# Kernel optimization log

Hardware: AMD Instinct MI355X
Metric: run time of the kernel (lower is better)

## Reference

```python
import jax, jax.numpy as jnp
import numpy as np

B, T, D = 16, 3000, 512
GROUPS, NUM_VARS = 2, 320
VQ_DIM = 256
VAR_DIM = VQ_DIM // GROUPS  # 128


def setup_inputs() -> dict:
    key = jax.random.key(0)
    k_x, k_w, k_v = jax.random.split(key, 3)
    x = jax.random.normal(k_x, (B, T, D), dtype=jnp.float32)
    # weight_proj: Linear(dim, groups*num_vars), weight ~ N(0,1), bias = 0
    W = jax.random.normal(k_w, (GROUPS * NUM_VARS, D), dtype=jnp.float32)
    b = jnp.zeros((GROUPS * NUM_VARS,), dtype=jnp.float32)
    # codebook: nn.init.uniform_ -> U[0,1); combine_groups=False -> num_groups = GROUPS
    codebook = jax.random.uniform(k_v, (1, GROUPS * NUM_VARS, VAR_DIM), dtype=jnp.float32)
    return {"x": x, "W": W, "b": b, "codebook": codebook}


def reference(x, W, b, codebook):
    """Eval-mode GumbelVectorQuantizer forward (hard argmax path).

    Returns (quantized [B,T,VQ_DIM], avg_probs [GROUPS, NUM_VARS]).
    """
    Bv, Tv, Dv = x.shape
    N = Bv * Tv
    # weight_proj
    logits = jnp.einsum('nd,vd->nv', x.reshape(N, Dv), W) + b  # [N, G*V]
    logits = logits.reshape(N, GROUPS, NUM_VARS)
    # hard one-hot over codebook entries per group
    k = jnp.argmax(logits, axis=-1)                             # [N, G] int
    hard = jax.nn.one_hot(k, NUM_VARS, dtype=logits.dtype)      # [N, G, V]
    # avg probs (softmax in fp32, mean over tokens)
    avg_probs = jax.nn.softmax(logits.astype(jnp.float32), axis=-1).mean(axis=0)  # [G, V]
    # dense multiply-sum against codebook == gather of selected code vectors
    vars_g = codebook.reshape(GROUPS, NUM_VARS, VAR_DIM)        # [G, V, d]
    out = jnp.einsum('ngv,gvd->ngd', hard, vars_g)              # [N, G, d]
    out = out.reshape(Bv, Tv, GROUPS * VAR_DIM)                 # [B, T, VQ_DIM]
    return out, avg_probs
```

## Files before the change

kernel.cpp:

```cpp
#include <hip/hip_runtime.h>

#define GROUPS 2
#define NUM_VARS 320
#define NVT 640
#define DIM 512
#define VAR_DIM 128
#define NTOK 48000
#define TM 32
#define TMF 64
#define BLOCK 256
#define KCH 256
#define XP 264
#define NT16 40
#define NKS 16
#define NTILE (NTOK / 16)
#define TSTRIDE (NKS * 2 * 512)

typedef short bf16x8 __attribute__((ext_vector_type(8)));
typedef float f32x4  __attribute__((ext_vector_type(4)));
typedef unsigned short u16;
typedef u16 u16x4 __attribute__((ext_vector_type(4)));
typedef u16 u16x8 __attribute__((ext_vector_type(8)));

__device__ inline u16 bf16_rne(float f) {
    unsigned u = __builtin_bit_cast(unsigned, f);
    return (u16)((u + 0x7fffu + ((u >> 16) & 1u)) >> 16);
}
__device__ inline void split2(float f, u16& h, u16& l) {
    h = bf16_rne(f);
    float fh = __builtin_bit_cast(float, (unsigned)h << 16);
    l = bf16_rne(f - fh);
}

__global__ void pack_w_kernel(const float* __restrict__ W, u16* __restrict__ Wpk) {
    int idx = blockIdx.x * blockDim.x + threadIdx.x;
    if (idx >= NT16 * NKS * 64 * 8) return;
    int j    = idx & 7;
    int lane = (idx >> 3) & 63;
    int ks   = (idx >> 9) & 15;
    int v16  = idx >> 13;
    int row  = v16 * 16 + (lane & 15);
    int k    = ks * 32 + 8 * (lane >> 4) + j;
    u16 h, l;
    split2(W[(size_t)row * DIM + k], h, l);
    size_t base = (size_t)((v16 * NKS + ks) * 2) * 512 + lane * 8 + j;
    Wpk[base]       = h;
    Wpk[base + 512] = l;
}

__global__ void split_x_pack_kernel(const float* __restrict__ x,
                                    u16* __restrict__ xpk) {
    const int gw   = (blockIdx.x * blockDim.x + threadIdx.x) >> 6;
    const int lane = threadIdx.x & 63;
    if (gw >= NTILE) return;
    const int l15 = lane & 15, l4 = lane >> 4;
    const float* xr = x + (size_t)(gw * 16 + l15) * DIM + 8 * l4;
    u16* dst = xpk + (size_t)gw * TSTRIDE + lane * 8;
#pragma unroll 4
    for (int ks = 0; ks < NKS; ++ks) {
        float4 a = *(const float4*)(xr + ks * 32);
        float4 b = *(const float4*)(xr + ks * 32 + 4);
        u16x8 hv, lv; u16 h, l;
        split2(a.x, h, l); hv[0] = h; lv[0] = l;
        split2(a.y, h, l); hv[1] = h; lv[1] = l;
        split2(a.z, h, l); hv[2] = h; lv[2] = l;
        split2(a.w, h, l); hv[3] = h; lv[3] = l;
        split2(b.x, h, l); hv[4] = h; lv[4] = l;
        split2(b.y, h, l); hv[5] = h; lv[5] = l;
        split2(b.z, h, l); hv[6] = h; lv[6] = l;
        split2(b.w, h, l); hv[7] = h; lv[7] = l;
        *(u16x8*)(dst + ks * 1024)       = hv;
        *(u16x8*)(dst + ks * 1024 + 512) = lv;
    }
}

__global__ __launch_bounds__(BLOCK, 2)
void vq_mfma_reg_kernel(const float* __restrict__ x,
                        const float* __restrict__ W,
                        const u16* __restrict__ xpk,
                        const u16* __restrict__ Wpk,
                        const float* __restrict__ bias,
                        const float* __restrict__ codebook,
                        float* __restrict__ out,
                        float* __restrict__ avg_out) {
    __shared__ float avg_s[NUM_VARS];
    __shared__ float tv_s[TMF][4][2];
    __shared__ int   ti_s[TMF][4][2];
    __shared__ float m_s[TMF], gap_s[TMF], sum_s[TMF];
    __shared__ int   i1_s[TMF], i2_s[TMF], kb_s[TMF];

    const int tid  = threadIdx.x;
    const int lane = tid & 63;
    const int ty   = tid >> 6;
    const int l15  = lane & 15;
    const int l4   = lane >> 4;
    const int g    = blockIdx.x & 1;
    const int n0   = (blockIdx.x >> 1) * TMF;

    for (int i = tid; i < NUM_VARS; i += BLOCK) avg_s[i] = 0.f;

    const f32x4 zf = {0.f, 0.f, 0.f, 0.f};
    f32x4 acc[4][5];
#pragma unroll
    for (int rt = 0; rt < 4; ++rt)
#pragma unroll
        for (int ct = 0; ct < 5; ++ct) acc[rt][ct] = zf;

    const u16* xa = xpk + (size_t)((blockIdx.x >> 1) * 4) * TSTRIDE + lane * 8;
    const u16* wpk_b = Wpk + (size_t)(g * 20 + ty * 5) * TSTRIDE + lane * 8;

#pragma unroll 2
    for (int ks = 0; ks < NKS; ++ks) {
        bf16x8 ah[4], al[4];
#pragma unroll
        for (int rt = 0; rt < 4; ++rt) {
            ah[rt] = *(const bf16x8*)(xa + (size_t)rt * TSTRIDE + ks * 1024);
            al[rt] = *(const bf16x8*)(xa + (size_t)rt * TSTRIDE + ks * 1024 + 512);
        }
#pragma unroll
        for (int ct = 0; ct < 5; ++ct) {
            const u16* wp = wpk_b + (size_t)(ct * NKS + ks) * 2 * 512;
            bf16x8 bh = *(const bf16x8*)wp;
            bf16x8 bl = *(const bf16x8*)(wp + 512);
#pragma unroll
            for (int rt = 0; rt < 4; ++rt) {
                acc[rt][ct] = __builtin_amdgcn_mfma_f32_16x16x32_bf16(ah[rt], bh, acc[rt][ct], 0, 0, 0);
                acc[rt][ct] = __builtin_amdgcn_mfma_f32_16x16x32_bf16(ah[rt], bl, acc[rt][ct], 0, 0, 0);
                acc[rt][ct] = __builtin_amdgcn_mfma_f32_16x16x32_bf16(al[rt], bh, acc[rt][ct], 0, 0, 0);
            }
        }
    }

#pragma unroll
    for (int ct = 0; ct < 5; ++ct) {
        float bv = bias[g * NUM_VARS + ty * 80 + ct * 16 + l15];
#pragma unroll
        for (int rt = 0; rt < 4; ++rt)
#pragma unroll
            for (int j = 0; j < 4; ++j) acc[rt][ct][j] += bv;
    }

#pragma unroll
    for (int rt = 0; rt < 4; ++rt)
#pragma unroll
    for (int j = 0; j < 4; ++j) {
        float v1 = -3.4e38f, v2 = -3.4e38f;
        int   i1 = 0x7fffffff, i2 = 0x7fffffff;
#pragma unroll
        for (int ct = 0; ct < 5; ++ct) {
            float val = acc[rt][ct][j];
            int   vi  = ty * 80 + ct * 16 + l15;
            if ((val > v1) || (val == v1 && vi < i1)) { v2 = v1; i2 = i1; v1 = val; i1 = vi; }
            else if ((val > v2) || (val == v2 && vi < i2)) { v2 = val; i2 = vi; }
        }
#pragma unroll
        for (int off = 1; off <= 8; off <<= 1) {
            float o1 = __shfl_xor(v1, off); int oi1 = __shfl_xor(i1, off);
            float o2 = __shfl_xor(v2, off); int oi2 = __shfl_xor(i2, off);
            if ((o1 > v1) || (o1 == v1 && oi1 < i1)) { v2 = v1; i2 = i1; v1 = o1; i1 = oi1; }
            else if ((o1 > v2) || (o1 == v2 && oi1 < i2)) { v2 = o1; i2 = oi1; }
            if ((o2 > v1) || (o2 == v1 && oi2 < i1)) { v2 = v1; i2 = i1; v1 = o2; i1 = oi2; }
            else if ((o2 > v2) || (o2 == v2 && oi2 < i2)) { v2 = o2; i2 = oi2; }
        }
        if (l15 == 0) {
            const int T = rt * 16 + l4 * 4 + j;
            tv_s[T][ty][0] = v1; tv_s[T][ty][1] = v2;
            ti_s[T][ty][0] = i1; ti_s[T][ty][1] = i2;
        }
    }
    __syncthreads();

    if (tid < TMF) {
        float v1 = -3.4e38f, v2 = -3.4e38f;
        int   i1 = 0x7fffffff, i2 = 0x7fffffff;
#pragma unroll
        for (int w = 0; w < 4; ++w)
#pragma unroll
            for (int q = 0; q < 2; ++q) {
                float val = tv_s[tid][w][q]; int vi = ti_s[tid][w][q];
                if ((val > v1) || (val == v1 && vi < i1)) { v2 = v1; i2 = i1; v1 = val; i1 = vi; }
                else if ((val > v2) || (val == v2 && vi < i2)) { v2 = val; i2 = vi; }
            }
        m_s[tid] = v1; gap_s[tid] = v1 - v2;
        i1_s[tid] = i1; i2_s[tid] = i2; kb_s[tid] = i1; sum_s[tid] = 0.f;
    }
    __syncthreads();

#pragma unroll
    for (int rt = 0; rt < 4; ++rt)
#pragma unroll
    for (int j = 0; j < 4; ++j) {
        const int T = rt * 16 + l4 * 4 + j;
        const float m = m_s[T];
        float s = 0.f;
#pragma unroll
        for (int ct = 0; ct < 5; ++ct) {
            float e = expf(acc[rt][ct][j] - m);
            acc[rt][ct][j] = e;
            s += e;
        }
#pragma unroll
        for (int off = 1; off <= 8; off <<= 1) s += __shfl_xor(s, off);
        if (l15 == 0) atomicAdd(&sum_s[T], s);
    }
    __syncthreads();

#pragma unroll
    for (int ct = 0; ct < 5; ++ct) {
        float tot = 0.f;
#pragma unroll
        for (int rt = 0; rt < 4; ++rt)
#pragma unroll
        for (int j = 0; j < 4; ++j) {
            const int T = rt * 16 + l4 * 4 + j;
            float v = acc[rt][ct][j] / sum_s[T];
            v += __shfl_xor(v, 16);
            v += __shfl_xor(v, 32);
            tot += v;
        }
        if (l4 == 0) avg_s[ty * 80 + ct * 16 + l15] += tot;
    }

    for (int t16 = 0; t16 < 16; ++t16) {
        const int T = ty * 16 + t16;
        if (gap_s[T] <= 0.05f) {
            const int i1 = i1_s[T], i2 = i2_s[T];
            const float* xr = x + (size_t)(n0 + T) * DIM;
            const float* w1 = W + (size_t)(g * NUM_VARS + i1) * DIM;
            const float* w2 = W + (size_t)(g * NUM_VARS + i2) * DIM;
            double d1 = 0.0, d2 = 0.0;
            for (int k = lane; k < DIM; k += 64) {
                double xv = (double)xr[k];
                d1 += xv * (double)w1[k];
                d2 += xv * (double)w2[k];
            }
#pragma unroll
            for (int off = 1; off <= 32; off <<= 1) {
                d1 += __shfl_xor(d1, off);
                d2 += __shfl_xor(d2, off);
            }
            d1 += (double)bias[g * NUM_VARS + i1];
            d2 += (double)bias[g * NUM_VARS + i2];
            if (lane == 0)
                kb_s[T] = (d2 > d1 || (d2 == d1 && i2 < i1)) ? i2 : i1;
        }
    }
    __syncthreads();

#pragma unroll
    for (int i = 0; i < 8; ++i) {
        const int f = tid + i * BLOCK;
        const int T = f >> 5, p = f & 31;
        const int kb = kb_s[T];
        float4 cv = *(const float4*)(codebook +
                     (size_t)(g * NUM_VARS + kb) * VAR_DIM + p * 4);
        *(float4*)(out + (size_t)(n0 + T) * (GROUPS * VAR_DIM) + g * VAR_DIM + p * 4) = cv;
    }

    const float scale = 1.f / (float)NTOK;
    for (int i = tid; i < NUM_VARS; i += BLOCK)
        atomicAdd(&avg_out[g * NUM_VARS + i], avg_s[i] * scale);
}

template <bool USE_WQ>
__global__ __launch_bounds__(BLOCK, 2)
void vq_mfma_kernel(const float* __restrict__ x,
                    const float* __restrict__ W,
                    const u16* __restrict__ Wpk,
                    const float* __restrict__ bias,
                    const float* __restrict__ codebook,
                    float* __restrict__ out,
                    float* __restrict__ avg_out) {
    __shared__ u16 xs_hi[TM][XP];
    __shared__ u16 xs_lo[TM][XP];
    __shared__ float avg_s[NUM_VARS];
    __shared__ float tv_s[TM][4][2];
    __shared__ int   ti_s[TM][4][2];
    __shared__ float m_s[TM], gap_s[TM], sum_s[TM];
    __shared__ int   i1_s[TM], i2_s[TM], kb_s[TM];

    const int tid  = threadIdx.x;
    const int lane = tid & 63;
    const int ty   = tid >> 6;
    const int l15  = lane & 15;
    const int l4   = lane >> 4;
    const int g    = blockIdx.x & 1;
    const int n0   = (blockIdx.x >> 1) * TM;

    for (int i = tid; i < NUM_VARS; i += BLOCK) avg_s[i] = 0.f;

    const f32x4 zf = {0.f, 0.f, 0.f, 0.f};
    f32x4 acc[2][5];
#pragma unroll
    for (int rt = 0; rt < 2; ++rt)
#pragma unroll
        for (int ct = 0; ct < 5; ++ct) acc[rt][ct] = zf;

    const int vw = g * NUM_VARS + ty * 80;

    for (int c = 0; c < DIM / KCH; ++c) {
        __syncthreads();
        {
            const int t  = tid >> 3;
            const int kb = (tid & 7) * 4;
            const float* xp = x + (size_t)(n0 + t) * DIM + c * KCH;
#pragma unroll
            for (int i = 0; i < 8; ++i) {
                const int k = kb + i * 32;
                float4 v = *(const float4*)(xp + k);
                u16x4 hv, lv; u16 h, l;
                split2(v.x, h, l); hv[0] = h; lv[0] = l;
                split2(v.y, h, l); hv[1] = h; lv[1] = l;
                split2(v.z, h, l); hv[2] = h; lv[2] = l;
                split2(v.w, h, l); hv[3] = h; lv[3] = l;
                *(u16x4*)&xs_hi[t][k] = hv;
                *(u16x4*)&xs_lo[t][k] = lv;
            }
        }
        __syncthreads();
#pragma unroll
        for (int ks = 0; ks < KCH / 32; ++ks) {
            const int ko = ks * 32 + 8 * l4;
            bf16x8 ah0 = *(const bf16x8*)&xs_hi[l15][ko];
            bf16x8 al0 = *(const bf16x8*)&xs_lo[l15][ko];
            bf16x8 ah1 = *(const bf16x8*)&xs_hi[16 + l15][ko];
            bf16x8 al1 = *(const bf16x8*)&xs_lo[16 + l15][ko];
            const int ksg = c * (KCH / 32) + ks;
#pragma unroll
            for (int ct = 0; ct < 5; ++ct) {
                bf16x8 bh, bl;
                if (USE_WQ) {
                    const int v16g = g * (NUM_VARS / 16) + ty * 5 + ct;
                    const u16* wp = Wpk + (size_t)((v16g * NKS + ksg) * 2) * 512 + lane * 8;
                    bh = *(const bf16x8*)wp;
                    bl = *(const bf16x8*)(wp + 512);
                } else {
                    const int kg = ksg * 32 + 8 * l4;
                    const float* wp = W + (size_t)(vw + ct * 16 + l15) * DIM + kg;
                    float4 wa = *(const float4*)wp;
                    float4 wb = *(const float4*)(wp + 4);
                    u16 h, l;
                    split2(wa.x, h, l); bh[0] = (short)h; bl[0] = (short)l;
                    split2(wa.y, h, l); bh[1] = (short)h; bl[1] = (short)l;
                    split2(wa.z, h, l); bh[2] = (short)h; bl[2] = (short)l;
                    split2(wa.w, h, l); bh[3] = (short)h; bl[3] = (short)l;
                    split2(wb.x, h, l); bh[4] = (short)h; bl[4] = (short)l;
                    split2(wb.y, h, l); bh[5] = (short)h; bl[5] = (short)l;
                    split2(wb.z, h, l); bh[6] = (short)h; bl[6] = (short)l;
                    split2(wb.w, h, l); bh[7] = (short)h; bl[7] = (short)l;
                }
                acc[0][ct] = __builtin_amdgcn_mfma_f32_16x16x32_bf16(ah0, bh, acc[0][ct], 0, 0, 0);
                acc[0][ct] = __builtin_amdgcn_mfma_f32_16x16x32_bf16(ah0, bl, acc[0][ct], 0, 0, 0);
                acc[0][ct] = __builtin_amdgcn_mfma_f32_16x16x32_bf16(al0, bh, acc[0][ct], 0, 0, 0);
                acc[1][ct] = __builtin_amdgcn_mfma_f32_16x16x32_bf16(ah1, bh, acc[1][ct], 0, 0, 0);
                acc[1][ct] = __builtin_amdgcn_mfma_f32_16x16x32_bf16(ah1, bl, acc[1][ct], 0, 0, 0);
                acc[1][ct] = __builtin_amdgcn_mfma_f32_16x16x32_bf16(al1, bh, acc[1][ct], 0, 0, 0);
            }
        }
    }

#pragma unroll
    for (int ct = 0; ct < 5; ++ct) {
        float bv = bias[vw + ct * 16 + l15];
#pragma unroll
        for (int rt = 0; rt < 2; ++rt)
#pragma unroll
            for (int j = 0; j < 4; ++j) acc[rt][ct][j] += bv;
    }

#pragma unroll
    for (int rt = 0; rt < 2; ++rt)
#pragma unroll
    for (int j = 0; j < 4; ++j) {
        float v1 = -3.4e38f, v2 = -3.4e38f;
        int   i1 = 0x7fffffff, i2 = 0x7fffffff;
#pragma unroll
        for (int ct = 0; ct < 5; ++ct) {
            float val = acc[rt][ct][j];
            int   vi  = ty * 80 + ct * 16 + l15;
            if ((val > v1) || (val == v1 && vi < i1)) { v2 = v1; i2 = i1; v1 = val; i1 = vi; }
            else if ((val > v2) || (val == v2 && vi < i2)) { v2 = val; i2 = vi; }
        }
#pragma unroll
        for (int off = 1; off <= 8; off <<= 1) {
            float o1 = __shfl_xor(v1, off); int oi1 = __shfl_xor(i1, off);
            float o2 = __shfl_xor(v2, off); int oi2 = __shfl_xor(i2, off);
            if ((o1 > v1) || (o1 == v1 && oi1 < i1)) { v2 = v1; i2 = i1; v1 = o1; i1 = oi1; }
            else if ((o1 > v2) || (o1 == v2 && oi1 < i2)) { v2 = o1; i2 = oi1; }
            if ((o2 > v1) || (o2 == v1 && oi2 < i1)) { v2 = v1; i2 = i1; v1 = o2; i1 = oi2; }
            else if ((o2 > v2) || (o2 == v2 && oi2 < i2)) { v2 = o2; i2 = oi2; }
        }
        if (l15 == 0) {
            const int T = rt * 16 + l4 * 4 + j;
            tv_s[T][ty][0] = v1; tv_s[T][ty][1] = v2;
            ti_s[T][ty][0] = i1; ti_s[T][ty][1] = i2;
        }
    }
    __syncthreads();

    if (tid < TM) {
        float v1 = -3.4e38f, v2 = -3.4e38f;
        int   i1 = 0x7fffffff, i2 = 0x7fffffff;
#pragma unroll
        for (int w = 0; w < 4; ++w)
#pragma unroll
            for (int q = 0; q < 2; ++q) {
                float val = tv_s[tid][w][q]; int vi = ti_s[tid][w][q];
                if ((val > v1) || (val == v1 && vi < i1)) { v2 = v1; i2 = i1; v1 = val; i1 = vi; }
                else if ((val > v2) || (val == v2 && vi < i2)) { v2 = val; i2 = vi; }
            }
        m_s[tid] = v1; gap_s[tid] = v1 - v2;
        i1_s[tid] = i1; i2_s[tid] = i2; kb_s[tid] = i1; sum_s[tid] = 0.f;
    }
    __syncthreads();

#pragma unroll
    for (int rt = 0; rt < 2; ++rt)
#pragma unroll
    for (int j = 0; j < 4; ++j) {
        const int T = rt * 16 + l4 * 4 + j;
        const float m = m_s[T];
        float s = 0.f;
#pragma unroll
        for (int ct = 0; ct < 5; ++ct) {
            float e = expf(acc[rt][ct][j] - m);
            acc[rt][ct][j] = e;
            s += e;
        }
#pragma unroll
        for (int off = 1; off <= 8; off <<= 1) s += __shfl_xor(s, off);
        if (l15 == 0) atomicAdd(&sum_s[T], s);
    }
    __syncthreads();

#pragma unroll
    for (int ct = 0; ct < 5; ++ct) {
        float tot = 0.f;
#pragma unroll
        for (int rt = 0; rt < 2; ++rt)
#pragma unroll
        for (int j = 0; j < 4; ++j) {
            const int T = rt * 16 + l4 * 4 + j;
            float v = acc[rt][ct][j] / sum_s[T];
            v += __shfl_xor(v, 16);
            v += __shfl_xor(v, 32);
            tot += v;
        }
        if (l4 == 0) avg_s[ty * 80 + ct * 16 + l15] += tot;
    }

    for (int t8 = 0; t8 < 8; ++t8) {
        const int T = ty * 8 + t8;
        if (gap_s[T] <= 0.05f) {
            const int i1 = i1_s[T], i2 = i2_s[T];
            const float* xr = x + (size_t)(n0 + T) * DIM;
            const float* w1 = W + (size_t)(g * NUM_VARS + i1) * DIM;
            const float* w2 = W + (size_t)(g * NUM_VARS + i2) * DIM;
            double d1 = 0.0, d2 = 0.0;
            for (int k = lane; k < DIM; k += 64) {
                double xv = (double)xr[k];
                d1 += xv * (double)w1[k];
                d2 += xv * (double)w2[k];
            }
#pragma unroll
            for (int off = 1; off <= 32; off <<= 1) {
                d1 += __shfl_xor(d1, off);
                d2 += __shfl_xor(d2, off);
            }
            d1 += (double)bias[g * NUM_VARS + i1];
            d2 += (double)bias[g * NUM_VARS + i2];
            if (lane == 0)
                kb_s[T] = (d2 > d1 || (d2 == d1 && i2 < i1)) ? i2 : i1;
        }
    }
    __syncthreads();

#pragma unroll
    for (int i = 0; i < 4; ++i) {
        const int f = tid + i * BLOCK;
        const int T = f >> 5, p = f & 31;
        const int kb = kb_s[T];
        float4 cv = *(const float4*)(codebook +
                     (size_t)(g * NUM_VARS + kb) * VAR_DIM + p * 4);
        *(float4*)(out + (size_t)(n0 + T) * (GROUPS * VAR_DIM) + g * VAR_DIM + p * 4) = cv;
    }

    const float scale = 1.f / (float)NTOK;
    for (int i = tid; i < NUM_VARS; i += BLOCK)
        atomicAdd(&avg_out[g * NUM_VARS + i], avg_s[i] * scale);
}

extern "C" void kernel_launch(void* const* d_in, const int* in_sizes, int n_in,
                              void* d_out, int out_size, void* d_ws, size_t ws_size,
                              hipStream_t stream) {
    const float* x  = (const float*)d_in[0];
    const float* W  = (const float*)d_in[1];
    const float* b  = (const float*)d_in[2];
    const float* cb = (const float*)d_in[3];
    float* out = (float*)d_out;
    float* avg = out + (size_t)NTOK * GROUPS * VAR_DIM;

    hipMemsetAsync(avg, 0, NVT * sizeof(float), stream);

    const size_t wpk_bytes = (size_t)NT16 * NKS * 2 * 512 * sizeof(u16);
    const size_t xpk_bytes = (size_t)NTILE * NKS * 2 * 512 * sizeof(u16);
    const size_t full_bytes = wpk_bytes + xpk_bytes;

    if (ws_size >= full_bytes) {
        u16* Wpk = (u16*)d_ws;
        u16* xpk = (u16*)((char*)d_ws + wpk_bytes);
        pack_w_kernel<<<(NT16 * NKS * 64 * 8 + 255) / 256, 256, 0, stream>>>(W, Wpk);
        split_x_pack_kernel<<<(NTILE + 3) / 4, 256, 0, stream>>>(x, xpk);
        vq_mfma_reg_kernel<<<(NTOK / TMF) * GROUPS, BLOCK, 0, stream>>>(
            x, W, xpk, Wpk, b, cb, out, avg);
    } else if (ws_size >= wpk_bytes) {
        u16* Wpk = (u16*)d_ws;
        pack_w_kernel<<<(NT16 * NKS * 64 * 8 + 255) / 256, 256, 0, stream>>>(W, Wpk);
        vq_mfma_kernel<true><<<(NTOK / TM) * GROUPS, BLOCK, 0, stream>>>(x, W, Wpk, b, cb, out, avg);
    } else {
        vq_mfma_kernel<false><<<(NTOK / TM) * GROUPS, BLOCK, 0, stream>>>(x, W, nullptr, b, cb, out, avg);
    }
}
```

Measured before the change: 200.6 us.

## Double token tile per block to 128 rows and hoist W fragments across row tiles

Result: slower. 300.8 us (+50.0%).

```diff
diff --git a/kernel.cpp b/kernel.cpp
--- a/kernel.cpp
+++ b/kernel.cpp
@@ -7,7 +7,7 @@
 #define VAR_DIM 128
 #define NTOK 48000
 #define TM 32
-#define TMF 64
+#define TMF 128
 #define BLOCK 256
 #define KCH 256
 #define XP 264
@@ -74,7 +74,7 @@
     }
 }
 
-__global__ __launch_bounds__(BLOCK, 2)
+__global__ __launch_bounds__(BLOCK, 1)
 void vq_mfma_reg_kernel(const float* __restrict__ x,
                         const float* __restrict__ W,
                         const u16* __restrict__ xpk,
@@ -100,33 +100,33 @@
     for (int i = tid; i < NUM_VARS; i += BLOCK) avg_s[i] = 0.f;
 
     const f32x4 zf = {0.f, 0.f, 0.f, 0.f};
-    f32x4 acc[4][5];
-#pragma unroll
-    for (int rt = 0; rt < 4; ++rt)
+    f32x4 acc[8][5];
+#pragma unroll
+    for (int rt = 0; rt < 8; ++rt)
 #pragma unroll
         for (int ct = 0; ct < 5; ++ct) acc[rt][ct] = zf;
 
-    const u16* xa = xpk + (size_t)((blockIdx.x >> 1) * 4) * TSTRIDE + lane * 8;
+    const u16* xa = xpk + (size_t)((blockIdx.x >> 1) * 8) * TSTRIDE + lane * 8;
     const u16* wpk_b = Wpk + (size_t)(g * 20 + ty * 5) * TSTRIDE + lane * 8;
 
 #pragma unroll 2
     for (int ks = 0; ks < NKS; ++ks) {
-        bf16x8 ah[4], al[4];
-#pragma unroll
-        for (int rt = 0; rt < 4; ++rt) {
-            ah[rt] = *(const bf16x8*)(xa + (size_t)rt * TSTRIDE + ks * 1024);
-            al[rt] = *(const bf16x8*)(xa + (size_t)rt * TSTRIDE + ks * 1024 + 512);
-        }
+        bf16x8 bh[5], bl[5];
 #pragma unroll
         for (int ct = 0; ct < 5; ++ct) {
-            const u16* wp = wpk_b + (size_t)(ct * NKS + ks) * 2 * 512;
-            bf16x8 bh = *(const bf16x8*)wp;
-            bf16x8 bl = *(const bf16x8*)(wp + 512);
-#pragma unroll
-            for (int rt = 0; rt < 4; ++rt) {
-                acc[rt][ct] = __builtin_amdgcn_mfma_f32_16x16x32_bf16(ah[rt], bh, acc[rt][ct], 0, 0, 0);
-                acc[rt][ct] = __builtin_amdgcn_mfma_f32_16x16x32_bf16(ah[rt], bl, acc[rt][ct], 0, 0, 0);
-                acc[rt][ct] = __builtin_amdgcn_mfma_f32_16x16x32_bf16(al[rt], bh, acc[rt][ct], 0, 0, 0);
+            const u16* wp = wpk_b + (size_t)(ct * NKS + ks) * 1024;
+            bh[ct] = *(const bf16x8*)wp;
+            bl[ct] = *(const bf16x8*)(wp + 512);
+        }
+#pragma unroll
+        for (int rt = 0; rt < 8; ++rt) {
+            bf16x8 ah = *(const bf16x8*)(xa + (size_t)rt * TSTRIDE + ks * 1024);
+            bf16x8 al = *(const bf16x8*)(xa + (size_t)rt * TSTRIDE + ks * 1024 + 512);
+#pragma unroll
+            for (int ct = 0; ct < 5; ++ct) {
+                acc[rt][ct] = __builtin_amdgcn_mfma_f32_16x16x32_bf16(ah, bh[ct], acc[rt][ct], 0, 0, 0);
+                acc[rt][ct] = __builtin_amdgcn_mfma_f32_16x16x32_bf16(ah, bl[ct], acc[rt][ct], 0, 0, 0);
+                acc[rt][ct] = __builtin_amdgcn_mfma_f32_16x16x32_bf16(al, bh[ct], acc[rt][ct], 0, 0, 0);
             }
         }
     }
@@ -135,13 +135,13 @@
     for (int ct = 0; ct < 5; ++ct) {
         float bv = bias[g * NUM_VARS + ty * 80 + ct * 16 + l15];
 #pragma unroll
-        for (int rt = 0; rt < 4; ++rt)
+        for (int rt = 0; rt < 8; ++rt)
 #pragma unroll
             for (int j = 0; j < 4; ++j) acc[rt][ct][j] += bv;
     }
 
 #pragma unroll
-    for (int rt = 0; rt < 4; ++rt)
+    for (int rt = 0; rt < 8; ++rt)
 #pragma unroll
     for (int j = 0; j < 4; ++j) {
         float v1 = -3.4e38f, v2 = -3.4e38f;
@@ -187,7 +187,7 @@
     __syncthreads();
 
 #pragma unroll
-    for (int rt = 0; rt < 4; ++rt)
+    for (int rt = 0; rt < 8; ++rt)
 #pragma unroll
     for (int j = 0; j < 4; ++j) {
         const int T = rt * 16 + l4 * 4 + j;
@@ -195,7 +195,7 @@
         float s = 0.f;
 #pragma unroll
         for (int ct = 0; ct < 5; ++ct) {
-            float e = expf(acc[rt][ct][j] - m);
+            float e = __expf(acc[rt][ct][j] - m);
             acc[rt][ct][j] = e;
             s += e;
         }
@@ -205,24 +205,36 @@
     }
     __syncthreads();
 
-#pragma unroll
-    for (int ct = 0; ct < 5; ++ct) {
-        float tot = 0.f;
-#pragma unroll
-        for (int rt = 0; rt < 4; ++rt)
+    {
+        float tot0 = 0.f, tot1 = 0.f, tot2 = 0.f, tot3 = 0.f, tot4 = 0.f;
+#pragma unroll
+        for (int rt = 0; rt < 8; ++rt)
 #pragma unroll
         for (int j = 0; j < 4; ++j) {
             const int T = rt * 16 + l4 * 4 + j;
-            float v = acc[rt][ct][j] / sum_s[T];
-            v += __shfl_xor(v, 16);
-            v += __shfl_xor(v, 32);
-            tot += v;
-        }
-        if (l4 == 0) avg_s[ty * 80 + ct * 16 + l15] += tot;
-    }
-
-    for (int t16 = 0; t16 < 16; ++t16) {
-        const int T = ty * 16 + t16;
+            const float inv = 1.f / sum_s[T];
+            float v0 = acc[rt][0][j] * inv;
+            float v1 = acc[rt][1][j] * inv;
+            float v2 = acc[rt][2][j] * inv;
+            float v3 = acc[rt][3][j] * inv;
+            float v4 = acc[rt][4][j] * inv;
+            v0 += __shfl_xor(v0, 16); v0 += __shfl_xor(v0, 32); tot0 += v0;
+            v1 += __shfl_xor(v1, 16); v1 += __shfl_xor(v1, 32); tot1 += v1;
+            v2 += __shfl_xor(v2, 16); v2 += __shfl_xor(v2, 32); tot2 += v2;
+            v3 += __shfl_xor(v3, 16); v3 += __shfl_xor(v3, 32); tot3 += v3;
+            v4 += __shfl_xor(v4, 16); v4 += __shfl_xor(v4, 32); tot4 += v4;
+        }
+        if (l4 == 0) {
+            avg_s[ty * 80 + 0 * 16 + l15] += tot0;
+            avg_s[ty * 80 + 1 * 16 + l15] += tot1;
+            avg_s[ty * 80 + 2 * 16 + l15] += tot2;
+            avg_s[ty * 80 + 3 * 16 + l15] += tot3;
+            avg_s[ty * 80 + 4 * 16 + l15] += tot4;
+        }
+    }
+
+    for (int t32 = 0; t32 < 32; ++t32) {
+        const int T = ty * 32 + t32;
         if (gap_s[T] <= 0.05f) {
             const int i1 = i1_s[T], i2 = i2_s[T];
             const float* xr = x + (size_t)(n0 + T) * DIM;
@@ -248,7 +260,7 @@
     __syncthreads();
 
 #pragma unroll
-    for (int i = 0; i < 8; ++i) {
+    for (int i = 0; i < 16; ++i) {
         const int f = tid + i * BLOCK;
         const int T = f >> 5, p = f & 31;
         const int kb = kb_s[T];
```

## Stage x tiles into LDS with async triple-buffered global_load_lds and fast softmax math

Applied to the files above, without the earlier changes.

After: 187.0 us. -6.8%, faster.

```diff
diff --git a/kernel.cpp b/kernel.cpp
--- a/kernel.cpp
+++ b/kernel.cpp
@@ -30,6 +30,13 @@
     h = bf16_rne(f);
     float fh = __builtin_bit_cast(float, (unsigned)h << 16);
     l = bf16_rne(f - fh);
+}
+
+__device__ __forceinline__ void gll16(const void* g, void* l) {
+    __builtin_amdgcn_global_load_lds(
+        (const __attribute__((address_space(1))) unsigned int*)g,
+        (__attribute__((address_space(3))) unsigned int*)l,
+        16, 0, 0);
 }
 
 __global__ void pack_w_kernel(const float* __restrict__ W, u16* __restrict__ Wpk) {
@@ -83,6 +90,7 @@
                         const float* __restrict__ codebook,
                         float* __restrict__ out,
                         float* __restrict__ avg_out) {
+    __shared__ u16 As[3][4][2][512];
     __shared__ float avg_s[NUM_VARS];
     __shared__ float tv_s[TMF][4][2];
     __shared__ int   ti_s[TMF][4][2];
@@ -106,29 +114,48 @@
 #pragma unroll
         for (int ct = 0; ct < 5; ++ct) acc[rt][ct] = zf;
 
-    const u16* xa = xpk + (size_t)((blockIdx.x >> 1) * 4) * TSTRIDE + lane * 8;
+    const u16* xa_st = xpk + (size_t)((blockIdx.x >> 1) * 4 + ty) * TSTRIDE + lane * 8;
     const u16* wpk_b = Wpk + (size_t)(g * 20 + ty * 5) * TSTRIDE + lane * 8;
 
-#pragma unroll 2
+    gll16(xa_st,        &As[0][ty][0][0]);
+    gll16(xa_st + 512,  &As[0][ty][1][0]);
+    gll16(xa_st + 1024, &As[1][ty][0][0]);
+    gll16(xa_st + 1536, &As[1][ty][1][0]);
+    asm volatile("s_waitcnt vmcnt(2)" ::: "memory");
+    __builtin_amdgcn_s_barrier();
+
+#pragma unroll 1
     for (int ks = 0; ks < NKS; ++ks) {
-        bf16x8 ah[4], al[4];
+        const int cur = ks % 3;
+        bf16x8 bh[5], bl[5];
+#pragma unroll
+        for (int ct = 0; ct < 5; ++ct) {
+            const u16* wp = wpk_b + (size_t)(ct * NKS + ks) * 1024;
+            bh[ct] = *(const bf16x8*)wp;
+            bl[ct] = *(const bf16x8*)(wp + 512);
+        }
 #pragma unroll
         for (int rt = 0; rt < 4; ++rt) {
-            ah[rt] = *(const bf16x8*)(xa + (size_t)rt * TSTRIDE + ks * 1024);
-            al[rt] = *(const bf16x8*)(xa + (size_t)rt * TSTRIDE + ks * 1024 + 512);
-        }
-#pragma unroll
-        for (int ct = 0; ct < 5; ++ct) {
-            const u16* wp = wpk_b + (size_t)(ct * NKS + ks) * 2 * 512;
-            bf16x8 bh = *(const bf16x8*)wp;
-            bf16x8 bl = *(const bf16x8*)(wp + 512);
-#pragma unroll
-            for (int rt = 0; rt < 4; ++rt) {
-                acc[rt][ct] = __builtin_amdgcn_mfma_f32_16x16x32_bf16(ah[rt], bh, acc[rt][ct], 0, 0, 0);
-                acc[rt][ct] = __builtin_amdgcn_mfma_f32_16x16x32_bf16(ah[rt], bl, acc[rt][ct], 0, 0, 0);
-                acc[rt][ct] = __builtin_amdgcn_mfma_f32_16x16x32_bf16(al[rt], bh, acc[rt][ct], 0, 0, 0);
-            }
-        }
+            bf16x8 ah = *(const bf16x8*)&As[cur][rt][0][lane * 8];
+            bf16x8 al = *(const bf16x8*)&As[cur][rt][1][lane * 8];
+#pragma unroll
+            for (int ct = 0; ct < 5; ++ct) {
+                acc[rt][ct] = __builtin_amdgcn_mfma_f32_16x16x32_bf16(ah, bh[ct], acc[rt][ct], 0, 0, 0);
+                acc[rt][ct] = __builtin_amdgcn_mfma_f32_16x16x32_bf16(ah, bl[ct], acc[rt][ct], 0, 0, 0);
+                acc[rt][ct] = __builtin_amdgcn_mfma_f32_16x16x32_bf16(al, bh[ct], acc[rt][ct], 0, 0, 0);
+            }
+        }
+        if (ks + 2 < NKS) {
+            const int nb = (ks + 2) % 3;
+            gll16(xa_st + (size_t)(ks + 2) * 1024,       &As[nb][ty][0][0]);
+            gll16(xa_st + (size_t)(ks + 2) * 1024 + 512, &As[nb][ty][1][0]);
+        }
+        if (ks < NKS - 2) {
+            asm volatile("s_waitcnt vmcnt(2) lgkmcnt(0)" ::: "memory");
+        } else {
+            asm volatile("s_waitcnt vmcnt(0) lgkmcnt(0)" ::: "memory");
+        }
+        __builtin_amdgcn_s_barrier();
     }
 
 #pragma unroll
@@ -195,7 +222,7 @@
         float s = 0.f;
 #pragma unroll
         for (int ct = 0; ct < 5; ++ct) {
-            float e = expf(acc[rt][ct][j] - m);
+            float e = __expf(acc[rt][ct][j] - m);
             acc[rt][ct][j] = e;
             s += e;
         }
@@ -213,7 +240,7 @@
 #pragma unroll
         for (int j = 0; j < 4; ++j) {
             const int T = rt * 16 + l4 * 4 + j;
-            float v = acc[rt][ct][j] / sum_s[T];
+            float v = acc[rt][ct][j] * (1.f / sum_s[T]);
             v += __shfl_xor(v, 16);
             v += __shfl_xor(v, 32);
             tot += v;
```
